# Performance work log

Measured on AMD Instinct MI355X. Metric: run time of the kernel, lower is better.

Reference implementation:

```python
import jax, jax.numpy as jnp
import numpy as np
import math

V, D, H, L, T_MAX = 512, 256, 4, 8, 256
HD = D // H
EPS = 1e-5


def _ln(x, g, b):
    mu = jnp.mean(x, axis=-1, keepdims=True)
    var = jnp.mean(jnp.square(x - mu), axis=-1, keepdims=True)
    return (x - mu) * jax.lax.rsqrt(var + EPS) * g + b


def _pos_encoding(T, D):
    pos = jnp.arange(T, dtype=jnp.float32)[:, None]
    div = jnp.exp(jnp.arange(0, D, 2, dtype=jnp.float32) * (-math.log(10000.0) / D))
    pe = jnp.zeros((T, D), dtype=jnp.float32)
    pe = pe.at[:, 0::2].set(jnp.sin(pos * div))
    pe = pe.at[:, 1::2].set(jnp.cos(pos * div))
    return pe


def setup_inputs() -> dict:
    key = jax.random.key(0)
    ks = jax.random.split(key, 16)
    s = 0.02
    B, T = 128, 256
    return {
        "idx": jax.random.randint(ks[0], (B, T), 0, V),
        "tok_emb": jax.random.normal(ks[1], (V, D)) * s,
        "Wq": jax.random.normal(ks[2], (L, D, D)) * s,
        "Wk": jax.random.normal(ks[3], (L, D, D)) * s,
        "Wv": jax.random.normal(ks[4], (L, D, D)) * s,
        "Wo": jax.random.normal(ks[5], (L, D, D)) * s,
        "bo": jnp.zeros((L, D)),
        "W1": jax.random.normal(ks[6], (L, D, D)) * s,
        "b1": jnp.zeros((L, D)),
        "W2": jax.random.normal(ks[7], (L, D, D)) * s,
        "b2": jnp.zeros((L, D)),
        "g1": jnp.ones((L, D)), "be1": jnp.zeros((L, D)),
        "g2": jnp.ones((L, D)), "be2": jnp.zeros((L, D)),
        "gf": jnp.ones((D,)), "bf": jnp.zeros((D,)),
        "Wh": jax.random.normal(ks[8], (D, V)) * s,
        "bh": jnp.zeros((V,)),
    }


def reference(idx, tok_emb, Wq, Wk, Wv, Wo, bo, W1, b1, W2, b2,
              g1, be1, g2, be2, gf, bf, Wh, bh):
    B, T = idx.shape
    x = tok_emb[idx] + _pos_encoding(T, D)[None]  # [B,T,D]
    causal = jnp.tril(jnp.ones((T, T), dtype=bool))
    scale = D ** (-0.5)  # NOTE: original scales by n_embd, not head_size
    for l in range(L):
        h = _ln(x, g1[l], be1[l])
        q = (h @ Wq[l]).reshape(B, T, H, HD)
        k = (h @ Wk[l]).reshape(B, T, H, HD)
        v = (h @ Wv[l]).reshape(B, T, H, HD)
        wei = jnp.einsum('bqhd,bkhd->bhqk', q, k) * scale
        wei = jnp.where(causal, wei, -jnp.inf)
        wei = jax.nn.softmax(wei, axis=-1)
        att = jnp.einsum('bhqk,bkhd->bqhd', wei, v).reshape(B, T, D)
        x = x + att @ Wo[l] + bo[l]
        h = _ln(x, g2[l], be2[l])
        x = x + jax.nn.relu(h @ W1[l] + b1[l]) @ W2[l] + b2[l]
    x = _ln(x, gf, bf)
    logits = x @ Wh + bh  # [B,T,V]
    return logits
```

## Files before the change

### kernel.cpp

```cpp
#include <hip/hip_runtime.h>
#include <hip/hip_bf16.h>

typedef unsigned short u16;
typedef __attribute__((ext_vector_type(8))) short short8;
typedef __attribute__((ext_vector_type(4))) float f32x4;

#define DEV static __device__ __forceinline__

DEV u16 f2bf(float x){
  union { __hip_bfloat16 b; u16 u; } c;
  c.b = __float2bfloat16(x);
  return c.u;
}

DEV void gload16(const void* g, void* lds){
  __builtin_amdgcn_global_load_lds((const __attribute__((address_space(1))) void*)g,
                                   (__attribute__((address_space(3))) void*)lds, 16, 0, 0);
}

__global__ __launch_bounds__(256)
void wconv_kernel(const float* __restrict__ Wq, const float* __restrict__ Wk,
                  const float* __restrict__ Wv, const float* __restrict__ Wo,
                  const float* __restrict__ W1, const float* __restrict__ W2,
                  const float* __restrict__ Wh,
                  u16* __restrict__ WqkvT, u16* __restrict__ WoT,
                  u16* __restrict__ W1T, u16* __restrict__ W2T, u16* __restrict__ WhT)
{
  __shared__ float tile[32][33];
  const int j = blockIdx.y;
  int N = 256;
  const float* src; u16* dst;
  if (j < 48){
    const int li = j / 6, t = j % 6;
    switch(t){
      case 0:  src = Wq + li*65536; dst = WqkvT + li*196608;          break;
      case 1:  src = Wk + li*65536; dst = WqkvT + li*196608 + 65536;  break;
      case 2:  src = Wv + li*65536; dst = WqkvT + li*196608 + 131072; break;
      case 3:  src = Wo + li*65536; dst = WoT  + li*65536;            break;
      case 4:  src = W1 + li*65536; dst = W1T  + li*65536;            break;
      default: src = W2 + li*65536; dst = W2T  + li*65536;            break;
    }
  } else { N = 512; src = Wh; dst = WhT; }
  const int tilesPerRow = N >> 5;
  if ((int)blockIdx.x >= tilesPerRow * 8) return;
  const int tx = blockIdx.x % tilesPerRow, ty = blockIdx.x / tilesPerRow;
  const int tid = threadIdx.x;
  const int r = tid >> 3, c4 = (tid & 7) * 4;
  float4 v = *(const float4*)(src + (size_t)(ty*32 + r)*N + tx*32 + c4);
  tile[r][c4+0]=v.x; tile[r][c4+1]=v.y; tile[r][c4+2]=v.z; tile[r][c4+3]=v.w;
  __syncthreads();
  ushort4 o;
  o.x = f2bf(tile[c4+0][r]); o.y = f2bf(tile[c4+1][r]);
  o.z = f2bf(tile[c4+2][r]); o.w = f2bf(tile[c4+3][r]);
  *(ushort4*)(dst + (size_t)(tx*32 + r)*256 + ty*32 + c4) = o;
}

__global__ __launch_bounds__(256)
void embed_kernel(const int* __restrict__ idx, const float* __restrict__ emb,
                  float* __restrict__ x)
{
  const int gid = blockIdx.x*256 + threadIdx.x;
  const int n = gid >> 6, c4 = (gid & 63) << 2;
  const int t = n & 255;
  const int v = idx[n];
  float4 e = *(const float4*)(emb + (size_t)v*256 + c4);
  float r[4];
  const float ef[4] = {e.x, e.y, e.z, e.w};
  #pragma unroll
  for (int i=0;i<4;++i){
    const int c = c4 + i;
    const float div = expf((float)(c & ~1) * (-9.210340371976184f/256.f));
    const float ang = (float)t * div;
    r[i] = ((c & 1) ? cosf(ang) : sinf(ang)) + ef[i];
  }
  float4 o = {r[0], r[1], r[2], r[3]};
  *(float4*)(x + (size_t)n*256 + c4) = o;
}

template<int PANELS, bool RELU_, bool OBF, bool BIAS_>
__global__ __launch_bounds__(256, 2)
void lngemm_kernel(const float* __restrict__ x, const float* __restrict__ g,
                   const float* __restrict__ b, const u16* __restrict__ W,
                   const float* __restrict__ bias, void* __restrict__ Cv, int ldC)
{
  __shared__ __align__(16) u16 Asw[32768];
  __shared__ __align__(16) u16 Bl[4096];
  const int tid = threadIdx.x;
  const int w = tid >> 6, l = tid & 63;
  const int lr = l & 15, lg = l >> 4;
  const int m0 = blockIdx.x * 128;
  const int wm = w >> 1, wn = w & 1;

  {
    const float4 gv = *(const float4*)(g + l*4);
    const float4 bv = *(const float4*)(b + l*4);
    #pragma unroll 4
    for (int i=0;i<32;++i){
      const int row = w*32 + i;
      const float4 v = *(const float4*)(x + (size_t)(m0+row)*256 + l*4);
      float s = v.x + v.y + v.z + v.w;
      float q = v.x*v.x + v.y*v.y + v.z*v.z + v.w*v.w;
      #pragma unroll
      for (int m=32; m; m>>=1){ s += __shfl_xor(s,m); q += __shfl_xor(q,m); }
      const float mu = s * (1.f/256.f);
      const float var = q * (1.f/256.f) - mu*mu;
      const float rstd = rsqrtf(var + 1e-5f);
      ushort4 o;
      o.x = f2bf((v.x-mu)*rstd*gv.x + bv.x);
      o.y = f2bf((v.y-mu)*rstd*gv.y + bv.y);
      o.z = f2bf((v.z-mu)*rstd*gv.z + bv.z);
      o.w = f2bf((v.w-mu)*rstd*gv.w + bv.w);
      *(ushort4*)((char*)Asw + row*512 + ((l*8) ^ ((row&7)<<4))) = o;
    }
  }
  __syncthreads();

  const int rowc = l >> 2;
  const int pswz = (l & 3) ^ ((l >> 3) & 3);

  #pragma unroll
  for (int p=0; p<PANELS; ++p){
    const int n0 = (blockIdx.y*PANELS + p) * 128;
    f32x4 acc[4][4];
    #pragma unroll
    for (int i=0;i<4;++i)
      #pragma unroll
      for (int jn=0;jn<4;++jn) acc[i][jn] = (f32x4){0.f,0.f,0.f,0.f};

    for (int kt=0; kt<8; ++kt){
      const int kofs = kt * 32;
      #pragma unroll
      for (int cc=0; cc<2; ++cc){
        const int c = w + cc*4;
        gload16(W + (size_t)(n0 + 16*c + rowc)*256 + kofs + pswz*8, &Bl[c*512]);
      }
      __syncthreads();
      short8 af[4], bf[4];
      #pragma unroll
      for (int mt=0; mt<4; ++mt){
        const int row = wm*64 + mt*16 + lr;
        af[mt] = *(const short8*)((const char*)Asw + row*512 +
                     ((kt*64 + lg*16) ^ ((row&7)<<4)));
      }
      #pragma unroll
      for (int nt=0; nt<4; ++nt){
        const int row = wn*64 + nt*16 + lr;
        const int kb = (lg*16) ^ ((((row>>1)&3))<<4);
        bf[nt] = *(const short8*)((const char*)Bl + row*64 + kb);
      }
      #pragma unroll
      for (int mt=0; mt<4; ++mt)
        #pragma unroll
        for (int nt=0; nt<4; ++nt)
          acc[mt][nt] = __builtin_amdgcn_mfma_f32_16x16x32_bf16(af[mt], bf[nt], acc[mt][nt], 0,0,0);
      __syncthreads();
    }

    #pragma unroll
    for (int nt=0; nt<4; ++nt){
      const int col = n0 + wn*64 + nt*16 + lr;
      const float bv = BIAS_ ? bias[col] : 0.f;
      #pragma unroll
      for (int mt=0; mt<4; ++mt){
        f32x4 v = acc[mt][nt];
        #pragma unroll
        for (int r=0;r<4;++r){
          const int row = m0 + wm*64 + mt*16 + lg*4 + r;
          float val = v[r] + bv;
          if (RELU_) val = fmaxf(val, 0.f);
          if (OBF) ((u16*)Cv)[(size_t)row*ldC + col] = f2bf(val);
          else     ((float*)Cv)[(size_t)row*ldC + col] = val;
        }
      }
    }
  }
}

template<bool OBF, bool RELU_, bool RES, bool BIAS_>
__global__ __launch_bounds__(256)
void gemm_kernel(const u16* __restrict__ A, const u16* __restrict__ W,
                 const float* __restrict__ bias, const float* __restrict__ resid,
                 void* __restrict__ Cv, int ldC)
{
  __shared__ __align__(16) u16 Al[4096];
  __shared__ __align__(16) u16 Bl[4096];
  const int tid = threadIdx.x;
  const int w = tid >> 6, l = tid & 63;
  const int lr = l & 15, lg = l >> 4;
  const int m0 = blockIdx.x * 128, n0 = blockIdx.y * 128;
  const int wm = w >> 1, wn = w & 1;

  f32x4 acc[4][4];
  #pragma unroll
  for (int i=0;i<4;++i)
    #pragma unroll
    for (int jn=0;jn<4;++jn) acc[i][jn] = (f32x4){0.f,0.f,0.f,0.f};

  const int rowc = l >> 2;
  const int pswz = (l & 3) ^ ((l >> 3) & 3);

  for (int kt=0; kt<8; ++kt){
    const int kofs = kt * 32;
    #pragma unroll
    for (int cc=0; cc<2; ++cc){
      const int c = w + cc*4;
      gload16(A + (size_t)(m0 + 16*c + rowc)*256 + kofs + pswz*8, &Al[c*512]);
      gload16(W + (size_t)(n0 + 16*c + rowc)*256 + kofs + pswz*8, &Bl[c*512]);
    }
    __syncthreads();
    short8 af[4], bf[4];
    #pragma unroll
    for (int mt=0; mt<4; ++mt){
      const int row = wm*64 + mt*16 + lr;
      const int kb = (lg*16) ^ ((((row>>1)&3))<<4);
      af[mt] = *(const short8*)((const char*)Al + row*64 + kb);
    }
    #pragma unroll
    for (int nt=0; nt<4; ++nt){
      const int row = wn*64 + nt*16 + lr;
      const int kb = (lg*16) ^ ((((row>>1)&3))<<4);
      bf[nt] = *(const short8*)((const char*)Bl + row*64 + kb);
    }
    #pragma unroll
    for (int mt=0; mt<4; ++mt)
      #pragma unroll
      for (int nt=0; nt<4; ++nt)
        acc[mt][nt] = __builtin_amdgcn_mfma_f32_16x16x32_bf16(af[mt], bf[nt], acc[mt][nt], 0,0,0);
    __syncthreads();
  }

  #pragma unroll
  for (int nt=0; nt<4; ++nt){
    const int col = n0 + wn*64 + nt*16 + lr;
    const float bv = BIAS_ ? bias[col] : 0.f;
    #pragma unroll
    for (int mt=0; mt<4; ++mt){
      f32x4 v = acc[mt][nt];
      #pragma unroll
      for (int r=0;r<4;++r){
        const int row = m0 + wm*64 + mt*16 + lg*4 + r;
        float val = v[r] + bv;
        if (RELU_) val = fmaxf(val, 0.f);
        if (RES)   val += resid[(size_t)row*256 + col];
        if (OBF) ((u16*)Cv)[(size_t)row*ldC + col] = f2bf(val);
        else     ((float*)Cv)[(size_t)row*ldC + col] = val;
      }
    }
  }
}

__global__ __launch_bounds__(512, 4)
void attn_kernel(const u16* __restrict__ qkv, u16* __restrict__ att)
{
  __shared__ __align__(16) u16 sK[16384];
  __shared__ __align__(16) u16 sV[16384];
  __shared__ __align__(16) u16 sP[8192];
  const int bh = blockIdx.x;
  const int b = bh >> 2, h = bh & 3;
  const int tid = threadIdx.x;
  const int w = tid >> 6, l = tid & 63, lr = l & 15, lg = l >> 4;
  const u16* base = qkv + (size_t)(b*256)*768;

  #pragma unroll
  for (int it=0; it<4; ++it){
    const int c = tid + it*512;
    const int t = c >> 3, p = c & 7;
    uint4 val = *(const uint4*)(base + (size_t)t*768 + 256 + h*64 + p*8);
    *(uint4*)((char*)sK + t*128 + ((p*16) ^ ((t&7)<<4))) = val;
  }
  #pragma unroll
  for (int it=0; it<8; ++it){
    const int c = tid + it*512;
    const int t = c >> 4, hdq = c & 15;
    ushort4 v = *(const ushort4*)(base + (size_t)t*768 + 512 + h*64 + hdq*4);
    #pragma unroll
    for (int j=0;j<4;++j){
      const int hd = hdq*4 + j;
      *(u16*)((char*)sV + hd*512 + ((t*2) ^ ((hd&31)<<4))) = ((const u16*)&v)[j];
    }
  }
  __syncthreads();

  char* sPw = (char*)sP + w*2048;
  const int swzq = (lr & 7) << 4;
  u16* ab = att + (size_t)(b*256)*256 + h*64;
  const float c1 = 0.09016844005556021f;

  #pragma unroll
  for (int ph=0; ph<2; ++ph){
    const int rt = ph ? (15 - w) : w;
    const u16* qp = base + (size_t)(rt*16 + lr)*768 + h*64;
    const short8 qf0 = *(const short8*)(qp + lg*8);
    const short8 qf1 = *(const short8*)(qp + 32 + lg*8);

    f32x4 acc[16];
    #pragma unroll
    for (int nt=0; nt<16; ++nt) acc[nt] = (f32x4){0.f,0.f,0.f,0.f};
    #pragma unroll
    for (int nt=0; nt<16; ++nt){
      if (nt <= rt){
        const int row = nt*16 + lr;
        const int swz = (row & 7) << 4;
        short8 k0 = *(const short8*)((const char*)sK + row*128 + ((lg*16) ^ swz));
        short8 k1 = *(const short8*)((const char*)sK + row*128 + ((64 + lg*16) ^ swz));
        acc[nt] = __builtin_amdgcn_mfma_f32_16x16x32_bf16(k0, qf0, acc[nt], 0,0,0);
        acc[nt] = __builtin_amdgcn_mfma_f32_16x16x32_bf16(k1, qf1, acc[nt], 0,0,0);
      }
    }
    #pragma unroll
    for (int nt=0; nt<16; ++nt){
      if (nt == rt){
        #pragma unroll
        for (int r=0;r<4;++r)
          acc[nt][r] = (lg*4 + r > lr) ? -3.0e38f : acc[nt][r];
      }
    }

    float m_ = -3.0e38f;
    #pragma unroll
    for (int nt=0; nt<16; ++nt){
      if (nt <= rt){
        float t01 = fmaxf(acc[nt][0], acc[nt][1]);
        float t23 = fmaxf(acc[nt][2], acc[nt][3]);
        m_ = fmaxf(m_, fmaxf(t01, t23));
      }
    }
    m_ = fmaxf(m_, __shfl_xor(m_, 16));
    m_ = fmaxf(m_, __shfl_xor(m_, 32));
    const float mm = m_ * c1;
    float s_ = 0.f;
    #pragma unroll
    for (int nt=0; nt<16; ++nt){
      if (nt <= rt){
        #pragma unroll
        for (int r=0;r<4;++r){
          const float p = exp2f(fmaf(acc[nt][r], c1, -mm));
          acc[nt][r] = p;
          s_ += p;
        }
      }
    }
    s_ += __shfl_xor(s_, 16);
    s_ += __shfl_xor(s_, 32);
    const float inv = 1.f / s_;

    f32x4 oacc[4];
    #pragma unroll
    for (int nt=0; nt<4; ++nt) oacc[nt] = (f32x4){0.f,0.f,0.f,0.f};
    #pragma unroll
    for (int c=0; c<4; ++c){
      if (c <= (rt >> 2)){
        #pragma unroll
        for (int e=0; e<4; ++e){
          const int nt = 4*c + e;
          ushort4 pk;
          #pragma unroll
          for (int r=0;r<4;++r){
            const float val = (nt <= rt) ? acc[nt][r] * inv : 0.f;
            ((u16*)&pk)[r] = f2bf(val);
          }
          *(ushort4*)(sPw + lr*128 + ((e*32 + lg*8) ^ swzq)) = pk;
        }
        #pragma unroll
        for (int kc=0; kc<2; ++kc){
          const int tc = 2*c + kc;
          if (tc <= (rt >> 1)){
            const short8 ap = *(const short8*)(sPw + lr*128 + ((kc*64 + lg*16) ^ swzq));
            #pragma unroll
            for (int nt=0; nt<4; ++nt){
              const int vrow = nt*16 + lr;
              const short8 bv = *(const short8*)((const char*)sV + vrow*512 +
                                   ((tc*64 + lg*16) ^ ((vrow&31)<<4)));
              oacc[nt] = __builtin_amdgcn_mfma_f32_16x16x32_bf16(ap, bv, oacc[nt], 0,0,0);
            }
          }
        }
      }
    }

    #pragma unroll
    for (int nt=0; nt<4; ++nt)
      #pragma unroll
      for (int r=0;r<4;++r){
        const int row = rt*16 + lg*4 + r;
        ab[(size_t)row*256 + nt*16 + lr] = f2bf(oacc[nt][r]);
      }
  }
}

extern "C" void kernel_launch(void* const* d_in, const int* in_sizes, int n_in,
                              void* d_out, int out_size, void* d_ws, size_t ws_size,
                              hipStream_t stream)
{
  (void)in_sizes; (void)n_in; (void)out_size; (void)ws_size;
  const int*   idx = (const int*)  d_in[0];
  const float* tok = (const float*)d_in[1];
  const float* Wq  = (const float*)d_in[2];
  const float* Wk  = (const float*)d_in[3];
  const float* Wv  = (const float*)d_in[4];
  const float* Wo  = (const float*)d_in[5];
  const float* bo  = (const float*)d_in[6];
  const float* W1  = (const float*)d_in[7];
  const float* b1  = (const float*)d_in[8];
  const float* W2  = (const float*)d_in[9];
  const float* b2  = (const float*)d_in[10];
  const float* g1  = (const float*)d_in[11];
  const float* be1 = (const float*)d_in[12];
  const float* g2  = (const float*)d_in[13];
  const float* be2 = (const float*)d_in[14];
  const float* gf  = (const float*)d_in[15];
  const float* bfi = (const float*)d_in[16];
  const float* Wh  = (const float*)d_in[17];
  const float* bh  = (const float*)d_in[18];

  char* ws = (char*)d_ws;
  float* x    = (float*)ws;  ws += (size_t)32768*256*4;
  u16*   hb   = (u16*)ws;    ws += (size_t)32768*256*2;
  u16*   qkv  = (u16*)ws;    ws += (size_t)32768*768*2;
  u16*   att  = (u16*)ws;    ws += (size_t)32768*256*2;
  u16*   WqkvT= (u16*)ws;    ws += (size_t)8*768*256*2;
  u16*   WoT  = (u16*)ws;    ws += (size_t)8*256*256*2;
  u16*   W1T  = (u16*)ws;    ws += (size_t)8*256*256*2;
  u16*   W2T  = (u16*)ws;    ws += (size_t)8*256*256*2;
  u16*   WhT  = (u16*)ws;    ws += (size_t)512*256*2;

  wconv_kernel<<<dim3(128,49),256,0,stream>>>(Wq,Wk,Wv,Wo,W1,W2,Wh,WqkvT,WoT,W1T,W2T,WhT);
  embed_kernel<<<8192,256,0,stream>>>(idx, tok, x);
  for (int l=0; l<8; ++l){
    lngemm_kernel<3,false,true,false><<<dim3(256,2),256,0,stream>>>(
        x, g1+l*256, be1+l*256, WqkvT + (size_t)l*196608, nullptr, qkv, 768);
    attn_kernel<<<512,512,0,stream>>>(qkv, att);
    gemm_kernel<false,false,true,true><<<dim3(256,2),256,0,stream>>>(
        att, WoT + (size_t)l*65536, bo + l*256, x, x, 256);
    lngemm_kernel<1,true,true,true><<<dim3(256,2),256,0,stream>>>(
        x, g2+l*256, be2+l*256, W1T + (size_t)l*65536, b1 + l*256, hb, 256);
    gemm_kernel<false,false,true,true><<<dim3(256,2),256,0,stream>>>(
        hb, W2T + (size_t)l*65536, b2 + l*256, x, x, 256);
  }
  lngemm_kernel<2,false,false,true><<<dim3(256,2),256,0,stream>>>(
      x, gf, bfi, WhT, bh, (float*)d_out, 512);
}
```

Measured before the change: 886.7 us.

## Fuse residual add and LayerNorm into GEMM epilogues, double-buffer GEMM loads

Moves LayerNorm out of the GEMM prologue and into the epilogue of the preceding GEMM: the Wo and W2 GEMMs now use full-row 64x256 tiles, add the residual, update x, and write a normalized bf16 activation for the next layer. The embedding kernel also applies the first LayerNorm. The plain GEMM gains double-buffered LDS tiles so the next k-slice loads while the current one computes. This removes the repeated fp32 x reads and per-panel LN recomputation in lngemm, at the cost of an extra intermediate buffer and a cross-wave LDS reduction for row statistics.

Measured after the change: 865.7 us. 1.02x faster.

```diff
diff --git a/kernel.cpp b/kernel.cpp
--- a/kernel.cpp
+++ b/kernel.cpp
@@ -56,13 +56,16 @@
 }
 
 __global__ __launch_bounds__(256)
-void embed_kernel(const int* __restrict__ idx, const float* __restrict__ emb,
-                  float* __restrict__ x)
+void embed_ln_kernel(const int* __restrict__ idx, const float* __restrict__ emb,
+                     const float* __restrict__ g, const float* __restrict__ be,
+                     float* __restrict__ x, u16* __restrict__ hb)
 {
-  const int gid = blockIdx.x*256 + threadIdx.x;
-  const int n = gid >> 6, c4 = (gid & 63) << 2;
-  const int t = n & 255;
-  const int v = idx[n];
+  const int tid = threadIdx.x;
+  const int w = tid >> 6, l = tid & 63;
+  const int row = blockIdx.x*4 + w;
+  const int t = row & 255;
+  const int v = idx[row];
+  const int c4 = l*4;
   float4 e = *(const float4*)(emb + (size_t)v*256 + c4);
   float r[4];
   const float ef[4] = {e.x, e.y, e.z, e.w};
@@ -73,153 +76,76 @@
     const float ang = (float)t * div;
     r[i] = ((c & 1) ? cosf(ang) : sinf(ang)) + ef[i];
   }
-  float4 o = {r[0], r[1], r[2], r[3]};
-  *(float4*)(x + (size_t)n*256 + c4) = o;
-}
-
-template<int PANELS, bool RELU_, bool OBF, bool BIAS_>
-__global__ __launch_bounds__(256, 2)
-void lngemm_kernel(const float* __restrict__ x, const float* __restrict__ g,
-                   const float* __restrict__ b, const u16* __restrict__ W,
-                   const float* __restrict__ bias, void* __restrict__ Cv, int ldC)
-{
-  __shared__ __align__(16) u16 Asw[32768];
-  __shared__ __align__(16) u16 Bl[4096];
-  const int tid = threadIdx.x;
-  const int w = tid >> 6, l = tid & 63;
-  const int lr = l & 15, lg = l >> 4;
-  const int m0 = blockIdx.x * 128;
-  const int wm = w >> 1, wn = w & 1;
-
-  {
-    const float4 gv = *(const float4*)(g + l*4);
-    const float4 bv = *(const float4*)(b + l*4);
-    #pragma unroll 4
-    for (int i=0;i<32;++i){
-      const int row = w*32 + i;
-      const float4 v = *(const float4*)(x + (size_t)(m0+row)*256 + l*4);
-      float s = v.x + v.y + v.z + v.w;
-      float q = v.x*v.x + v.y*v.y + v.z*v.z + v.w*v.w;
-      #pragma unroll
-      for (int m=32; m; m>>=1){ s += __shfl_xor(s,m); q += __shfl_xor(q,m); }
-      const float mu = s * (1.f/256.f);
-      const float var = q * (1.f/256.f) - mu*mu;
-      const float rstd = rsqrtf(var + 1e-5f);
-      ushort4 o;
-      o.x = f2bf((v.x-mu)*rstd*gv.x + bv.x);
-      o.y = f2bf((v.y-mu)*rstd*gv.y + bv.y);
-      o.z = f2bf((v.z-mu)*rstd*gv.z + bv.z);
-      o.w = f2bf((v.w-mu)*rstd*gv.w + bv.w);
-      *(ushort4*)((char*)Asw + row*512 + ((l*8) ^ ((row&7)<<4))) = o;
-    }
-  }
-  __syncthreads();
-
-  const int rowc = l >> 2;
-  const int pswz = (l & 3) ^ ((l >> 3) & 3);
-
-  #pragma unroll
-  for (int p=0; p<PANELS; ++p){
-    const int n0 = (blockIdx.y*PANELS + p) * 128;
-    f32x4 acc[4][4];
-    #pragma unroll
-    for (int i=0;i<4;++i)
-      #pragma unroll
-      for (int jn=0;jn<4;++jn) acc[i][jn] = (f32x4){0.f,0.f,0.f,0.f};
-
-    for (int kt=0; kt<8; ++kt){
-      const int kofs = kt * 32;
-      #pragma unroll
-      for (int cc=0; cc<2; ++cc){
-        const int c = w + cc*4;
-        gload16(W + (size_t)(n0 + 16*c + rowc)*256 + kofs + pswz*8, &Bl[c*512]);
-      }
-      __syncthreads();
-      short8 af[4], bf[4];
-      #pragma unroll
-      for (int mt=0; mt<4; ++mt){
-        const int row = wm*64 + mt*16 + lr;
-        af[mt] = *(const short8*)((const char*)Asw + row*512 +
-                     ((kt*64 + lg*16) ^ ((row&7)<<4)));
-      }
-      #pragma unroll
-      for (int nt=0; nt<4; ++nt){
-        const int row = wn*64 + nt*16 + lr;
-        const int kb = (lg*16) ^ ((((row>>1)&3))<<4);
-        bf[nt] = *(const short8*)((const char*)Bl + row*64 + kb);
-      }
-      #pragma unroll
-      for (int mt=0; mt<4; ++mt)
-        #pragma unroll
-        for (int nt=0; nt<4; ++nt)
-          acc[mt][nt] = __builtin_amdgcn_mfma_f32_16x16x32_bf16(af[mt], bf[nt], acc[mt][nt], 0,0,0);
-      __syncthreads();
-    }
-
-    #pragma unroll
-    for (int nt=0; nt<4; ++nt){
-      const int col = n0 + wn*64 + nt*16 + lr;
-      const float bv = BIAS_ ? bias[col] : 0.f;
-      #pragma unroll
-      for (int mt=0; mt<4; ++mt){
-        f32x4 v = acc[mt][nt];
-        #pragma unroll
-        for (int r=0;r<4;++r){
-          const int row = m0 + wm*64 + mt*16 + lg*4 + r;
-          float val = v[r] + bv;
-          if (RELU_) val = fmaxf(val, 0.f);
-          if (OBF) ((u16*)Cv)[(size_t)row*ldC + col] = f2bf(val);
-          else     ((float*)Cv)[(size_t)row*ldC + col] = val;
-        }
-      }
-    }
-  }
-}
-
-template<bool OBF, bool RELU_, bool RES, bool BIAS_>
+  *(float4*)(x + (size_t)row*256 + c4) = (float4){r[0],r[1],r[2],r[3]};
+  float s = r[0]+r[1]+r[2]+r[3];
+  float q = r[0]*r[0]+r[1]*r[1]+r[2]*r[2]+r[3]*r[3];
+  #pragma unroll
+  for (int m=32; m; m>>=1){ s += __shfl_xor(s,m); q += __shfl_xor(q,m); }
+  const float mu = s * (1.f/256.f);
+  const float var = q * (1.f/256.f) - mu*mu;
+  const float rstd = rsqrtf(var + 1e-5f);
+  const float4 gv = *(const float4*)(g + c4);
+  const float4 bv = *(const float4*)(be + c4);
+  ushort4 o;
+  o.x = f2bf((r[0]-mu)*rstd*gv.x + bv.x);
+  o.y = f2bf((r[1]-mu)*rstd*gv.y + bv.y);
+  o.z = f2bf((r[2]-mu)*rstd*gv.z + bv.z);
+  o.w = f2bf((r[3]-mu)*rstd*gv.w + bv.w);
+  *(ushort4*)(hb + (size_t)row*256 + c4) = o;
+}
+
+template<bool OBF, bool RELU_, bool BIAS_>
 __global__ __launch_bounds__(256)
 void gemm_kernel(const u16* __restrict__ A, const u16* __restrict__ W,
-                 const float* __restrict__ bias, const float* __restrict__ resid,
-                 void* __restrict__ Cv, int ldC)
+                 const float* __restrict__ bias, void* __restrict__ Cv, int ldC)
 {
-  __shared__ __align__(16) u16 Al[4096];
-  __shared__ __align__(16) u16 Bl[4096];
+  __shared__ __align__(16) u16 Al[2][4096];
+  __shared__ __align__(16) u16 Bl[2][4096];
   const int tid = threadIdx.x;
   const int w = tid >> 6, l = tid & 63;
   const int lr = l & 15, lg = l >> 4;
   const int m0 = blockIdx.x * 128, n0 = blockIdx.y * 128;
   const int wm = w >> 1, wn = w & 1;
-
-  f32x4 acc[4][4];
-  #pragma unroll
-  for (int i=0;i<4;++i)
-    #pragma unroll
-    for (int jn=0;jn<4;++jn) acc[i][jn] = (f32x4){0.f,0.f,0.f,0.f};
-
   const int rowc = l >> 2;
   const int pswz = (l & 3) ^ ((l >> 3) & 3);
 
+  f32x4 acc[4][4];
+  #pragma unroll
+  for (int i=0;i<4;++i)
+    #pragma unroll
+    for (int jn=0;jn<4;++jn) acc[i][jn] = (f32x4){0.f,0.f,0.f,0.f};
+
+  #pragma unroll
+  for (int cc=0; cc<2; ++cc){
+    const int c = w + cc*4;
+    gload16(A + (size_t)(m0 + 16*c + rowc)*256 + pswz*8, &Al[0][c*512]);
+    gload16(W + (size_t)(n0 + 16*c + rowc)*256 + pswz*8, &Bl[0][c*512]);
+  }
+  __syncthreads();
+
   for (int kt=0; kt<8; ++kt){
-    const int kofs = kt * 32;
-    #pragma unroll
-    for (int cc=0; cc<2; ++cc){
-      const int c = w + cc*4;
-      gload16(A + (size_t)(m0 + 16*c + rowc)*256 + kofs + pswz*8, &Al[c*512]);
-      gload16(W + (size_t)(n0 + 16*c + rowc)*256 + kofs + pswz*8, &Bl[c*512]);
-    }
-    __syncthreads();
+    if (kt < 7){
+      const int kofs = (kt+1) * 32, nb = (kt+1) & 1;
+      #pragma unroll
+      for (int cc=0; cc<2; ++cc){
+        const int c = w + cc*4;
+        gload16(A + (size_t)(m0 + 16*c + rowc)*256 + kofs + pswz*8, &Al[nb][c*512]);
+        gload16(W + (size_t)(n0 + 16*c + rowc)*256 + kofs + pswz*8, &Bl[nb][c*512]);
+      }
+    }
+    const int buf = kt & 1;
     short8 af[4], bf[4];
     #pragma unroll
     for (int mt=0; mt<4; ++mt){
       const int row = wm*64 + mt*16 + lr;
       const int kb = (lg*16) ^ ((((row>>1)&3))<<4);
-      af[mt] = *(const short8*)((const char*)Al + row*64 + kb);
+      af[mt] = *(const short8*)((const char*)Al[buf] + row*64 + kb);
     }
     #pragma unroll
     for (int nt=0; nt<4; ++nt){
       const int row = wn*64 + nt*16 + lr;
       const int kb = (lg*16) ^ ((((row>>1)&3))<<4);
-      bf[nt] = *(const short8*)((const char*)Bl + row*64 + kb);
+      bf[nt] = *(const short8*)((const char*)Bl[buf] + row*64 + kb);
     }
     #pragma unroll
     for (int mt=0; mt<4; ++mt)
@@ -241,12 +167,144 @@
         const int row = m0 + wm*64 + mt*16 + lg*4 + r;
         float val = v[r] + bv;
         if (RELU_) val = fmaxf(val, 0.f);
-        if (RES)   val += resid[(size_t)row*256 + col];
         if (OBF) ((u16*)Cv)[(size_t)row*ldC + col] = f2bf(val);
         else     ((float*)Cv)[(size_t)row*ldC + col] = val;
       }
     }
   }
+}
+
+__global__ __launch_bounds__(256, 2)
+void gemm_res_ln_kernel(const u16* __restrict__ A, const u16* __restrict__ W,
+                        const float* __restrict__ bias,
+                        const float* __restrict__ g, const float* __restrict__ be,
+                        float* __restrict__ x, u16* __restrict__ hb)
+{
+  __shared__ __align__(16) u16 Al[2][2048];
+  __shared__ __align__(16) u16 Bl[2][8192];
+  __shared__ float sS[64][2], sQ[64][2];
+  const int tid = threadIdx.x;
+  const int w = tid >> 6, l = tid & 63;
+  const int lr = l & 15, lg = l >> 4;
+  const int m0 = blockIdx.x * 64;
+  const int wm = w >> 1, wn = w & 1;
+  const int rowc = l >> 2;
+  const int pswz = (l & 3) ^ ((l >> 3) & 3);
+
+  f32x4 acc[2][2][4];
+  #pragma unroll
+  for (int p=0;p<2;++p)
+    #pragma unroll
+    for (int i=0;i<2;++i)
+      #pragma unroll
+      for (int jn=0;jn<4;++jn) acc[p][i][jn] = (f32x4){0.f,0.f,0.f,0.f};
+
+  gload16(A + (size_t)(m0 + 16*w + rowc)*256 + pswz*8, &Al[0][w*512]);
+  #pragma unroll
+  for (int cc=0; cc<4; ++cc){
+    const int c = w + cc*4;
+    gload16(W + (size_t)(16*c + rowc)*256 + pswz*8, &Bl[0][c*512]);
+  }
+  __syncthreads();
+
+  for (int kt=0; kt<8; ++kt){
+    if (kt < 7){
+      const int kofs = (kt+1)*32, nb = (kt+1)&1;
+      gload16(A + (size_t)(m0 + 16*w + rowc)*256 + kofs + pswz*8, &Al[nb][w*512]);
+      #pragma unroll
+      for (int cc=0; cc<4; ++cc){
+        const int c = w + cc*4;
+        gload16(W + (size_t)(16*c + rowc)*256 + kofs + pswz*8, &Bl[nb][c*512]);
+      }
+    }
+    const int buf = kt & 1;
+    short8 af[2], bf[2][4];
+    #pragma unroll
+    for (int mt=0; mt<2; ++mt){
+      const int row = wm*32 + mt*16 + lr;
+      const int kb = (lg*16) ^ ((((row>>1)&3))<<4);
+      af[mt] = *(const short8*)((const char*)Al[buf] + row*64 + kb);
+    }
+    #pragma unroll
+    for (int p=0; p<2; ++p)
+      #pragma unroll
+      for (int nt=0; nt<4; ++nt){
+        const int brow = p*128 + wn*64 + nt*16 + lr;
+        const int kb = (lg*16) ^ ((((brow>>1)&3))<<4);
+        bf[p][nt] = *(const short8*)((const char*)Bl[buf] + brow*64 + kb);
+      }
+    #pragma unroll
+    for (int p=0; p<2; ++p)
+      #pragma unroll
+      for (int mt=0; mt<2; ++mt)
+        #pragma unroll
+        for (int nt=0; nt<4; ++nt)
+          acc[p][mt][nt] = __builtin_amdgcn_mfma_f32_16x16x32_bf16(af[mt], bf[p][nt], acc[p][mt][nt], 0,0,0);
+    __syncthreads();
+  }
+
+  float bcol[2][4], gcol[2][4], becol[2][4];
+  #pragma unroll
+  for (int p=0;p<2;++p)
+    #pragma unroll
+    for (int nt=0;nt<4;++nt){
+      const int col = p*128 + wn*64 + nt*16 + lr;
+      bcol[p][nt] = bias[col]; gcol[p][nt] = g[col]; becol[p][nt] = be[col];
+    }
+  float s8[2][4], q8[2][4];
+  #pragma unroll
+  for (int mt=0;mt<2;++mt)
+    #pragma unroll
+    for (int rr=0;rr<4;++rr){ s8[mt][rr]=0.f; q8[mt][rr]=0.f; }
+
+  #pragma unroll
+  for (int p=0;p<2;++p)
+    #pragma unroll
+    for (int mt=0;mt<2;++mt)
+      #pragma unroll
+      for (int nt=0;nt<4;++nt)
+        #pragma unroll
+        for (int rr=0;rr<4;++rr){
+          const int row = m0 + wm*32 + mt*16 + lg*4 + rr;
+          const int col = p*128 + wn*64 + nt*16 + lr;
+          float val = acc[p][mt][nt][rr] + bcol[p][nt] + x[(size_t)row*256 + col];
+          x[(size_t)row*256 + col] = val;
+          acc[p][mt][nt][rr] = val;
+          s8[mt][rr] += val; q8[mt][rr] += val*val;
+        }
+  #pragma unroll
+  for (int mt=0;mt<2;++mt)
+    #pragma unroll
+    for (int rr=0;rr<4;++rr){
+      #pragma unroll
+      for (int m=1; m<16; m<<=1){
+        s8[mt][rr] += __shfl_xor(s8[mt][rr], m);
+        q8[mt][rr] += __shfl_xor(q8[mt][rr], m);
+      }
+      if (lr == 0){
+        const int lrow = wm*32 + mt*16 + lg*4 + rr;
+        sS[lrow][wn] = s8[mt][rr]; sQ[lrow][wn] = q8[mt][rr];
+      }
+    }
+  __syncthreads();
+
+  #pragma unroll
+  for (int mt=0;mt<2;++mt)
+    #pragma unroll
+    for (int rr=0;rr<4;++rr){
+      const int lrow = wm*32 + mt*16 + lg*4 + rr;
+      const float mu = (sS[lrow][0] + sS[lrow][1]) * (1.f/256.f);
+      const float var = (sQ[lrow][0] + sQ[lrow][1]) * (1.f/256.f) - mu*mu;
+      const float rstd = rsqrtf(var + 1e-5f);
+      #pragma unroll
+      for (int p=0;p<2;++p)
+        #pragma unroll
+        for (int nt=0;nt<4;++nt){
+          const int col = p*128 + wn*64 + nt*16 + lr;
+          const float out = (acc[p][mt][nt][rr] - mu)*rstd*gcol[p][nt] + becol[p][nt];
+          hb[(size_t)(m0+lrow)*256 + col] = f2bf(out);
+        }
+    }
 }
 
 __global__ __launch_bounds__(512, 4)
@@ -416,6 +474,7 @@
   char* ws = (char*)d_ws;
   float* x    = (float*)ws;  ws += (size_t)32768*256*4;
   u16*   hb   = (u16*)ws;    ws += (size_t)32768*256*2;
+  u16*   mid  = (u16*)ws;    ws += (size_t)32768*256*2;
   u16*   qkv  = (u16*)ws;    ws += (size_t)32768*768*2;
   u16*   att  = (u16*)ws;    ws += (size_t)32768*256*2;
   u16*   WqkvT= (u16*)ws;    ws += (size_t)8*768*256*2;
@@ -425,18 +484,20 @@
   u16*   WhT  = (u16*)ws;    ws += (size_t)512*256*2;
 
   wconv_kernel<<<dim3(128,49),256,0,stream>>>(Wq,Wk,Wv,Wo,W1,W2,Wh,WqkvT,WoT,W1T,W2T,WhT);
-  embed_kernel<<<8192,256,0,stream>>>(idx, tok, x);
+  embed_ln_kernel<<<8192,256,0,stream>>>(idx, tok, g1, be1, x, hb);
   for (int l=0; l<8; ++l){
-    lngemm_kernel<3,false,true,false><<<dim3(256,2),256,0,stream>>>(
-        x, g1+l*256, be1+l*256, WqkvT + (size_t)l*196608, nullptr, qkv, 768);
+    gemm_kernel<true,false,false><<<dim3(256,6),256,0,stream>>>(
+        hb, WqkvT + (size_t)l*196608, nullptr, qkv, 768);
     attn_kernel<<<512,512,0,stream>>>(qkv, att);
-    gemm_kernel<false,false,true,true><<<dim3(256,2),256,0,stream>>>(
-        att, WoT + (size_t)l*65536, bo + l*256, x, x, 256);
-    lngemm_kernel<1,true,true,true><<<dim3(256,2),256,0,stream>>>(
-        x, g2+l*256, be2+l*256, W1T + (size_t)l*65536, b1 + l*256, hb, 256);
-    gemm_kernel<false,false,true,true><<<dim3(256,2),256,0,stream>>>(
-        hb, W2T + (size_t)l*65536, b2 + l*256, x, x, 256);
-  }
-  lngemm_kernel<2,false,false,true><<<dim3(256,2),256,0,stream>>>(
-      x, gf, bfi, WhT, bh, (float*)d_out, 512);
-}
+    gemm_res_ln_kernel<<<512,256,0,stream>>>(
+        att, WoT + (size_t)l*65536, bo + l*256, g2 + l*256, be2 + l*256, x, hb);
+    gemm_kernel<true,true,true><<<dim3(256,2),256,0,stream>>>(
+        hb, W1T + (size_t)l*65536, b1 + l*256, mid, 256);
+    const float* gn = (l < 7) ? (g1 + (l+1)*256) : gf;
+    const float* bn = (l < 7) ? (be1 + (l+1)*256) : bfi;
+    gemm_res_ln_kernel<<<512,256,0,stream>>>(
+        mid, W2T + (size_t)l*65536, b2 + l*256, gn, bn, x, hb);
+  }
+  gemm_kernel<false,false,true><<<dim3(256,4),256,0,stream>>>(
+      hb, WhT, bh, (float*)d_out, 512);
+}
```
